# Kernel optimization log

Measured on AMD Instinct MI355X. Metric: run time of the kernel, lower is better.

The kernel has to match this reference:

```python
import jax, jax.numpy as jnp
import numpy as np

NUM_EXPERTS = 64
TOP_K = 2
B, S, EMB, MLP = 4, 2048, 1024, 2048


def setup_inputs() -> dict:
    key = jax.random.key(0)
    k1, k2, k3, k4, k5 = jax.random.split(key, 5)
    inputs = jax.random.normal(k1, (B, S, EMB), dtype=jnp.float32)
    gate_kernel = jax.random.normal(k2, (EMB, NUM_EXPERTS), dtype=jnp.float32) / np.sqrt(EMB)
    w0 = jax.random.normal(k3, (NUM_EXPERTS, EMB, MLP), dtype=jnp.float32) / np.sqrt(EMB)
    w1 = jax.random.normal(k4, (NUM_EXPERTS, EMB, MLP), dtype=jnp.float32) / np.sqrt(EMB)
    wo = jax.random.normal(k5, (NUM_EXPERTS, MLP, EMB), dtype=jnp.float32) / np.sqrt(MLP)
    return {"inputs": inputs, "gate_kernel": gate_kernel, "w0": w0, "w1": w1, "wo": wo}


def reference(inputs, gate_kernel, w0, w1, wo):
    b, s, e = inputs.shape
    x = inputs.reshape(b * s, e)                                  # [T, E]
    # Router (DenseGeneral gate)
    gate_logits = jnp.einsum('te,ex->tx', x, gate_kernel)         # [T, X]
    # permute(): top-k gating + sort tokens by expert
    weights, selected = jax.lax.top_k(gate_logits, TOP_K)         # [T, K]
    weights = jax.nn.softmax(weights.astype(jnp.float32), axis=-1)
    flat_experts = selected.reshape(-1)                           # [T*K]
    sort_idx = jnp.argsort(flat_experts)                          # [T*K]
    token_idx = sort_idx // TOP_K
    sorted_x = jnp.take(x, token_idx, axis=0)                     # [T*K, E]
    group_sizes = jnp.bincount(flat_experts, length=NUM_EXPERTS).astype(jnp.int32)
    # grouped GEMMs (gated FFN: silu(x@w0) * (x@w1) @ wo)
    h0 = jax.lax.ragged_dot(sorted_x, w0, group_sizes)            # [T*K, M]
    h1 = jax.lax.ragged_dot(sorted_x, w1, group_sizes)            # [T*K, M]
    inter = jax.nn.silu(h0) * h1
    out_sorted = jax.lax.ragged_dot(inter, wo, group_sizes)       # [T*K, E]
    # unpermute(): restore token order, weighted combine over top-k
    unsorted = jnp.take(out_sorted, jnp.argsort(sort_idx), axis=0)
    per_tok = unsorted.reshape(b * s, TOP_K, e)
    out = jnp.einsum('BKE,BK->BE', per_tok.astype(jnp.float32), weights)
    return out.reshape(b, s, e)
```

## Files before the change

kernel.cpp:

```cpp
#include <hip/hip_runtime.h>
#include <hip/hip_bf16.h>
#include <math.h>

#define NTOK   8192
#define NEXP   64
#define EMBD   1024
#define MLPD   2048
#define TOPK   2
#define NFLAT  (NTOK * TOPK)
#define BKD    32
#define MAXCH  8

typedef __attribute__((ext_vector_type(4)))  float  f32x4;
typedef __attribute__((ext_vector_type(16))) float  f32x16;
typedef __attribute__((ext_vector_type(8)))  __bf16 bf16x8;

__device__ __forceinline__ void gl16(const void* g, void* lds_base) {
  __builtin_amdgcn_global_load_lds(
      (const __attribute__((address_space(1))) unsigned int*)g,
      (__attribute__((address_space(3))) unsigned int*)lds_base, 16, 0, 0);
}
__device__ __forceinline__ void vm0_bar() {
  asm volatile("s_waitcnt vmcnt(0)" ::: "memory");
  __builtin_amdgcn_s_barrier();
}
__device__ __forceinline__ void lgkm0_bar() {
  asm volatile("s_waitcnt lgkmcnt(0)" ::: "memory");
  __builtin_amdgcn_sched_barrier(0);
  __builtin_amdgcn_s_barrier();
}

#define OFF_COUNTS 0
#define OFF_BASE   256
#define OFF_RUN    512
#define OFF_EFLAT  1024
#define OFF_WFLAT  (1024 + 65536)
#define OFF_ROWTOK (1024 + 2 * 65536)
#define OFF_F2R    (1024 + 3 * 65536)
#define OFF_INTER  (1024 + 4 * 65536)
#define OFF_OS     (OFF_INTER + (size_t)NFLAT * MLPD * 2)
#define NEED_F32   (OFF_OS + (size_t)NFLAT * EMBD * 4)

__global__ __launch_bounds__(256) void router_topk(
    const float* __restrict__ x, const float* __restrict__ gk,
    int* __restrict__ e_flat, float* __restrict__ w_flat) {
  int t = blockIdx.x * 4 + (threadIdx.x >> 6);
  int l = threadIdx.x & 63;
  const float* xr = x + (size_t)t * EMBD;
  float acc = 0.f;
  #pragma unroll 8
  for (int i = 0; i < EMBD; ++i)
    acc = fmaf(xr[i], gk[i * NEXP + l], acc);
  float m = acc;
  for (int o = 32; o; o >>= 1) m = fmaxf(m, __shfl_xor(m, o));
  unsigned long long b1 = __ballot(acc == m);
  int i1 = __ffsll(b1) - 1;
  float v2 = (l == i1) ? -INFINITY : acc;
  float m2 = v2;
  for (int o = 32; o; o >>= 1) m2 = fmaxf(m2, __shfl_xor(m2, o));
  unsigned long long b2 = __ballot(v2 == m2);
  int i2 = __ffsll(b2) - 1;
  if (l == 0) {
    float e2 = expf(m2 - m);
    float inv = 1.f / (1.f + e2);
    e_flat[2 * t] = i1;  e_flat[2 * t + 1] = i2;
    w_flat[2 * t] = inv; w_flat[2 * t + 1] = e2 * inv;
  }
}

__global__ void hist_k(const int* __restrict__ ef, int* __restrict__ counts) {
  int j = blockIdx.x * 256 + threadIdx.x;
  if (j < NFLAT) atomicAdd(&counts[ef[j]], 1);
}

__global__ void scan_k(const int* __restrict__ counts, int* __restrict__ base) {
  if (threadIdx.x == 0) {
    int s = 0;
    for (int e = 0; e < NEXP; ++e) { base[e] = s; s += counts[e]; }
  }
}

__global__ void scatter_k(const int* __restrict__ ef, const int* __restrict__ base,
                          int* __restrict__ run, int* __restrict__ rowtok,
                          int* __restrict__ f2r) {
  int j = blockIdx.x * 256 + threadIdx.x;
  if (j < NFLAT) {
    int e = ef[j];
    int r = base[e] + atomicAdd(&run[e], 1);
    f2r[j] = r;
    rowtok[r] = j >> 1;
  }
}

__global__ __launch_bounds__(256, 3) void gemm1_k(
    const float* __restrict__ x, const float* __restrict__ w0,
    const float* __restrict__ w1, const int* __restrict__ counts,
    const int* __restrict__ base, const int* __restrict__ rowtok,
    __hip_bfloat16* __restrict__ inter) {
  int e = blockIdx.z;
  int Me = counts[e];
  int mc = blockIdx.y;
  if (mc * 128 >= Me) return;
  int rs = base[e];
  int nb = blockIdx.x * 64;
  int t = threadIdx.x;
  int wv = t >> 6, l = t & 63;
  int wr = wv >> 1, wc = wv & 1;
  int lo = l & 31, hi = l >> 5;

  __shared__ float Ash[4096];
  __shared__ float Bsh[2 * 2048];

  const float* abase0 = x;
  const float* abase1 = x;
  const float* wbase  = w0;
  if (wv < 2) {
    int g0 = wv * 2, g1 = wv * 2 + 1;
    int r0 = mc * 128 + g0 * 32 + lo; r0 = r0 < Me ? r0 : Me - 1;
    int r1 = mc * 128 + g1 * 32 + lo; r1 = r1 < Me ? r1 : Me - 1;
    abase0 = x + (size_t)rowtok[rs + r0] * EMBD + hi * 4;
    abase1 = x + (size_t)rowtok[rs + r1] * EMBD + hi * 4;
  } else {
    const float* w = (wv == 3) ? w1 : w0;
    wbase = w + (size_t)e * EMBD * MLPD + nb + (l & 15) * 4 + (size_t)(l >> 4) * MLPD;
  }
  int matofs = (wv & 1) * 2048;

  auto STAGE = [&](int kk) {
    if (wv < 2) {
      #pragma unroll
      for (int h = 0; h < 4; ++h) {
        gl16(abase0 + kk + h * 8, &Ash[((wv * 2 + 0) * 4 + h) * 256]);
        gl16(abase1 + kk + h * 8, &Ash[((wv * 2 + 1) * 4 + h) * 256]);
      }
    } else {
      #pragma unroll
      for (int j = 0; j < 8; ++j)
        gl16(wbase + (size_t)(kk + j * 4) * MLPD, &Bsh[matofs + j * 256]);
    }
  };

  f32x16 acc0[2], acc1[2];
  #pragma unroll
  for (int g = 0; g < 2; ++g)
    #pragma unroll
    for (int r = 0; r < 16; ++r) { acc0[g][r] = 0.f; acc1[g][r] = 0.f; }

  STAGE(0);
  const int NT = EMBD / BKD;
  for (int ks = 0; ks < NT; ++ks) {
    vm0_bar();
    f32x4 a[2][2][2];
    #pragma unroll
    for (int g = 0; g < 2; ++g)
      #pragma unroll
      for (int kh = 0; kh < 2; ++kh) {
        int idx = (((wr * 2 + g) * 4 + kh * 2 + hi) * 256) + lo * 4;
        a[g][kh][0] = *(const f32x4*)&Ash[idx];
        a[g][kh][1] = *(const f32x4*)&Ash[idx + 128];
      }
    float b[2][2][8];
    #pragma unroll
    for (int m = 0; m < 2; ++m)
      #pragma unroll
      for (int kh = 0; kh < 2; ++kh) {
        int bi = m * 2048 + (kh * 16 + hi * 8) * 64 + wc * 32 + lo;
        #pragma unroll
        for (int q = 0; q < 8; ++q) b[m][kh][q] = Bsh[bi + q * 64];
      }
    lgkm0_bar();
    if (ks + 1 < NT) STAGE((ks + 1) * BKD);
    bf16x8 av[2][2], bv[2][2];
    #pragma unroll
    for (int g = 0; g < 2; ++g)
      #pragma unroll
      for (int kh = 0; kh < 2; ++kh) {
        #pragma unroll
        for (int q = 0; q < 4; ++q) {
          av[g][kh][q]     = (__bf16)a[g][kh][0][q];
          av[g][kh][4 + q] = (__bf16)a[g][kh][1][q];
        }
      }
    #pragma unroll
    for (int m = 0; m < 2; ++m)
      #pragma unroll
      for (int kh = 0; kh < 2; ++kh)
        #pragma unroll
        for (int q = 0; q < 8; ++q) bv[m][kh][q] = (__bf16)b[m][kh][q];
    #pragma unroll
    for (int kh = 0; kh < 2; ++kh)
      #pragma unroll
      for (int g = 0; g < 2; ++g) {
        acc0[g] = __builtin_amdgcn_mfma_f32_32x32x16_bf16(av[g][kh], bv[0][kh], acc0[g], 0, 0, 0);
        acc1[g] = __builtin_amdgcn_mfma_f32_32x32x16_bf16(av[g][kh], bv[1][kh], acc1[g], 0, 0, 0);
      }
  }

  #pragma unroll
  for (int g = 0; g < 2; ++g)
    #pragma unroll
    for (int r = 0; r < 16; ++r) {
      int rl = mc * 128 + wr * 64 + g * 32 + (r & 3) + 8 * (r >> 2) + 4 * hi;
      if (rl < Me) {
        float h0 = acc0[g][r], h1 = acc1[g][r];
        float s = h0 / (1.f + expf(-h0)) * h1;
        inter[(size_t)(rs + rl) * MLPD + nb + wc * 32 + lo] = (__hip_bfloat16)s;
      }
    }
}

template <typename OS_T>
__global__ __launch_bounds__(256, 4) void gemm2_k(
    const __hip_bfloat16* __restrict__ inter, const float* __restrict__ wo,
    const int* __restrict__ counts, const int* __restrict__ base,
    OS_T* __restrict__ os) {
  int e = blockIdx.z;
  int Me = counts[e];
  int mc = blockIdx.y;
  if (mc * 128 >= Me) return;
  int rs = base[e];
  int nb = blockIdx.x * 64;
  int t = threadIdx.x;
  int wv = t >> 6, l = t & 63;
  int wr = wv >> 1, wc = wv & 1;
  int lo = l & 31, hi = l >> 5;

  __shared__ __bf16 A2[4096];
  __shared__ float  B2[2048];

  const __hip_bfloat16* ab0 = inter;
  const __hip_bfloat16* ab1 = inter;
  const float* wbase = wo;
  if (wv < 2) {
    int g0 = wv * 2, g1 = wv * 2 + 1;
    int r0 = mc * 128 + g0 * 32 + lo; r0 = r0 < Me ? r0 : Me - 1;
    int r1 = mc * 128 + g1 * 32 + lo; r1 = r1 < Me ? r1 : Me - 1;
    ab0 = inter + (size_t)(rs + r0) * MLPD + hi * 8;
    ab1 = inter + (size_t)(rs + r1) * MLPD + hi * 8;
  } else {
    wbase = wo + (size_t)e * MLPD * EMBD + nb + (l & 15) * 4 + (size_t)(l >> 4) * EMBD;
  }
  int jofs = (wv & 1) * 4;

  auto STAGE = [&](int kk) {
    if (wv < 2) {
      #pragma unroll
      for (int kh = 0; kh < 2; ++kh) {
        gl16(ab0 + kk + kh * 16, &A2[((wv * 2 + 0) * 2 + kh) * 512]);
        gl16(ab1 + kk + kh * 16, &A2[((wv * 2 + 1) * 2 + kh) * 512]);
      }
    } else {
      #pragma unroll
      for (int j = 0; j < 4; ++j)
        gl16(wbase + (size_t)(kk + (jofs + j) * 4) * EMBD, &B2[(jofs + j) * 256]);
    }
  };

  f32x16 acc[2];
  #pragma unroll
  for (int g = 0; g < 2; ++g)
    #pragma unroll
    for (int r = 0; r < 16; ++r) acc[g][r] = 0.f;

  STAGE(0);
  const int NT = MLPD / BKD;
  for (int ks = 0; ks < NT; ++ks) {
    vm0_bar();
    bf16x8 av[2][2];
    #pragma unroll
    for (int g = 0; g < 2; ++g)
      #pragma unroll
      for (int kh = 0; kh < 2; ++kh)
        av[g][kh] = *(const bf16x8*)&A2[(((wr * 2 + g) * 2 + kh) * 512) + l * 8];
    float b[2][8];
    #pragma unroll
    for (int kh = 0; kh < 2; ++kh) {
      int bi = (kh * 16 + hi * 8) * 64 + wc * 32 + lo;
      #pragma unroll
      for (int q = 0; q < 8; ++q) b[kh][q] = B2[bi + q * 64];
    }
    lgkm0_bar();
    if (ks + 1 < NT) STAGE((ks + 1) * BKD);
    bf16x8 bv[2];
    #pragma unroll
    for (int kh = 0; kh < 2; ++kh)
      #pragma unroll
      for (int q = 0; q < 8; ++q) bv[kh][q] = (__bf16)b[kh][q];
    #pragma unroll
    for (int kh = 0; kh < 2; ++kh)
      #pragma unroll
      for (int g = 0; g < 2; ++g)
        acc[g] = __builtin_amdgcn_mfma_f32_32x32x16_bf16(av[g][kh], bv[kh], acc[g], 0, 0, 0);
  }

  #pragma unroll
  for (int g = 0; g < 2; ++g)
    #pragma unroll
    for (int r = 0; r < 16; ++r) {
      int rl = mc * 128 + wr * 64 + g * 32 + (r & 3) + 8 * (r >> 2) + 4 * hi;
      if (rl < Me)
        os[(size_t)(rs + rl) * EMBD + nb + wc * 32 + lo] = (OS_T)acc[g][r];
    }
}

template <typename OS_T>
__global__ __launch_bounds__(256) void combine_k(
    const OS_T* __restrict__ os, const int* __restrict__ f2r,
    const float* __restrict__ wf, float* __restrict__ out) {
  int t = blockIdx.x;
  int c = threadIdx.x * 4;
  int r0 = f2r[2 * t], r1 = f2r[2 * t + 1];
  float wa = wf[2 * t], wb = wf[2 * t + 1];
  const OS_T* pa = os + (size_t)r0 * EMBD + c;
  const OS_T* pb = os + (size_t)r1 * EMBD + c;
  float4 o;
  o.x = wa * (float)pa[0] + wb * (float)pb[0];
  o.y = wa * (float)pa[1] + wb * (float)pb[1];
  o.z = wa * (float)pa[2] + wb * (float)pb[2];
  o.w = wa * (float)pa[3] + wb * (float)pb[3];
  *(float4*)(out + (size_t)t * EMBD + c) = o;
}

extern "C" void kernel_launch(void* const* d_in, const int* in_sizes, int n_in,
                              void* d_out, int out_size, void* d_ws, size_t ws_size,
                              hipStream_t stream) {
  const float* x  = (const float*)d_in[0];
  const float* gk = (const float*)d_in[1];
  const float* w0 = (const float*)d_in[2];
  const float* w1 = (const float*)d_in[3];
  const float* wo = (const float*)d_in[4];
  float* out = (float*)d_out;
  char* ws = (char*)d_ws;

  int*   counts = (int*)(ws + OFF_COUNTS);
  int*   basep  = (int*)(ws + OFF_BASE);
  int*   run    = (int*)(ws + OFF_RUN);
  int*   ef     = (int*)(ws + OFF_EFLAT);
  float* wfl    = (float*)(ws + OFF_WFLAT);
  int*   rowtok = (int*)(ws + OFF_ROWTOK);
  int*   f2r    = (int*)(ws + OFF_F2R);
  __hip_bfloat16* inter = (__hip_bfloat16*)(ws + OFF_INTER);

  hipMemsetAsync(ws, 0, 1024, stream);
  router_topk<<<NTOK / 4, 256, 0, stream>>>(x, gk, ef, wfl);
  hist_k<<<NFLAT / 256, 256, 0, stream>>>(ef, counts);
  scan_k<<<1, 64, 0, stream>>>(counts, basep);
  scatter_k<<<NFLAT / 256, 256, 0, stream>>>(ef, basep, run, rowtok, f2r);
  gemm1_k<<<dim3(MLPD / 64, MAXCH, NEXP), 256, 0, stream>>>(x, w0, w1, counts, basep, rowtok, inter);

  if (ws_size >= NEED_F32) {
    float* os = (float*)(ws + OFF_OS);
    gemm2_k<float><<<dim3(EMBD / 64, MAXCH, NEXP), 256, 0, stream>>>(inter, wo, counts, basep, os);
    combine_k<float><<<NTOK, 256, 0, stream>>>(os, f2r, wfl, out);
  } else {
    __hip_bfloat16* os = (__hip_bfloat16*)(ws + OFF_OS);
    gemm2_k<__hip_bfloat16><<<dim3(EMBD / 64, MAXCH, NEXP), 256, 0, stream>>>(inter, wo, counts, basep, os);
    combine_k<__hip_bfloat16><<<NTOK, 256, 0, stream>>>(os, f2r, wfl, out);
  }
}
```

Measured before the change: 1.098 ms.

## Double-buffer weight tiles in LDS with partial vmcnt waits in both GEMMs

Adds a second LDS buffer for the weight tiles in gemm1, and for both the A and B tiles in gemm2, and prefetches two K-steps ahead. Waits become partial (vmcnt(8) or vmcnt(4)) instead of a full drain, so global-to-LDS loads for the next tile overlap the current step's compute. The cost is more LDS per block, which may lower occupancy (gemm1's B buffer grows to 32KB). The per-wave vmcnt counting also has to stay correct for the prefetch to be safe.

```diff
diff --git a/kernel.cpp b/kernel.cpp
--- a/kernel.cpp
+++ b/kernel.cpp
@@ -19,10 +19,6 @@
   __builtin_amdgcn_global_load_lds(
       (const __attribute__((address_space(1))) unsigned int*)g,
       (__attribute__((address_space(3))) unsigned int*)lds_base, 16, 0, 0);
-}
-__device__ __forceinline__ void vm0_bar() {
-  asm volatile("s_waitcnt vmcnt(0)" ::: "memory");
-  __builtin_amdgcn_s_barrier();
 }
 __device__ __forceinline__ void lgkm0_bar() {
   asm volatile("s_waitcnt lgkmcnt(0)" ::: "memory");
@@ -109,7 +105,7 @@
   int lo = l & 31, hi = l >> 5;
 
   __shared__ float Ash[4096];
-  __shared__ float Bsh[2 * 2048];
+  __shared__ float Bsh[2][4096];
 
   const float* abase0 = x;
   const float* abase1 = x;
@@ -126,18 +122,17 @@
   }
   int matofs = (wv & 1) * 2048;
 
-  auto STAGE = [&](int kk) {
-    if (wv < 2) {
-      #pragma unroll
-      for (int h = 0; h < 4; ++h) {
-        gl16(abase0 + kk + h * 8, &Ash[((wv * 2 + 0) * 4 + h) * 256]);
-        gl16(abase1 + kk + h * 8, &Ash[((wv * 2 + 1) * 4 + h) * 256]);
-      }
-    } else {
-      #pragma unroll
-      for (int j = 0; j < 8; ++j)
-        gl16(wbase + (size_t)(kk + j * 4) * MLPD, &Bsh[matofs + j * 256]);
-    }
+  auto STAGE_A = [&](int kk) {
+    #pragma unroll
+    for (int h = 0; h < 4; ++h) {
+      gl16(abase0 + kk + h * 8, &Ash[((wv * 2 + 0) * 4 + h) * 256]);
+      gl16(abase1 + kk + h * 8, &Ash[((wv * 2 + 1) * 4 + h) * 256]);
+    }
+  };
+  auto STAGE_B = [&](int buf, int kk) {
+    #pragma unroll
+    for (int j = 0; j < 8; ++j)
+      gl16(wbase + (size_t)(kk + j * 4) * MLPD, &Bsh[buf][matofs + j * 256]);
   };
 
   f32x16 acc0[2], acc1[2];
@@ -146,10 +141,15 @@
     #pragma unroll
     for (int r = 0; r < 16; ++r) { acc0[g][r] = 0.f; acc1[g][r] = 0.f; }
 
-  STAGE(0);
+  if (wv < 2) STAGE_A(0);
+  else { STAGE_B(0, 0); STAGE_B(1, BKD); }
+
   const int NT = EMBD / BKD;
   for (int ks = 0; ks < NT; ++ks) {
-    vm0_bar();
+    if (wv >= 2 && ks + 1 < NT) asm volatile("s_waitcnt vmcnt(8)" ::: "memory");
+    else                        asm volatile("s_waitcnt vmcnt(0)" ::: "memory");
+    __builtin_amdgcn_s_barrier();
+
     f32x4 a[2][2][2];
     #pragma unroll
     for (int g = 0; g < 2; ++g)
@@ -160,27 +160,29 @@
         a[g][kh][1] = *(const f32x4*)&Ash[idx + 128];
       }
     float b[2][2][8];
+    const float* bb = Bsh[ks & 1];
     #pragma unroll
     for (int m = 0; m < 2; ++m)
       #pragma unroll
       for (int kh = 0; kh < 2; ++kh) {
         int bi = m * 2048 + (kh * 16 + hi * 8) * 64 + wc * 32 + lo;
         #pragma unroll
-        for (int q = 0; q < 8; ++q) b[m][kh][q] = Bsh[bi + q * 64];
+        for (int q = 0; q < 8; ++q) b[m][kh][q] = bb[bi + q * 64];
       }
     lgkm0_bar();
-    if (ks + 1 < NT) STAGE((ks + 1) * BKD);
+    if (wv < 2) { if (ks + 1 < NT) STAGE_A((ks + 1) * BKD); }
+    else if (ks + 2 < NT) STAGE_B(ks & 1, (ks + 2) * BKD);
+
     bf16x8 av[2][2], bv[2][2];
     #pragma unroll
     for (int g = 0; g < 2; ++g)
       #pragma unroll
-      for (int kh = 0; kh < 2; ++kh) {
+      for (int kh = 0; kh < 2; ++kh)
         #pragma unroll
         for (int q = 0; q < 4; ++q) {
           av[g][kh][q]     = (__bf16)a[g][kh][0][q];
           av[g][kh][4 + q] = (__bf16)a[g][kh][1][q];
         }
-      }
     #pragma unroll
     for (int m = 0; m < 2; ++m)
       #pragma unroll
@@ -225,8 +227,8 @@
   int wr = wv >> 1, wc = wv & 1;
   int lo = l & 31, hi = l >> 5;
 
-  __shared__ __bf16 A2[4096];
-  __shared__ float  B2[2048];
+  __shared__ __bf16 A2[2][4096];
+  __shared__ float  B2[2][2048];
 
   const __hip_bfloat16* ab0 = inter;
   const __hip_bfloat16* ab1 = inter;
@@ -242,17 +244,17 @@
   }
   int jofs = (wv & 1) * 4;
 
-  auto STAGE = [&](int kk) {
+  auto STAGE = [&](int buf, int kk) {
     if (wv < 2) {
       #pragma unroll
       for (int kh = 0; kh < 2; ++kh) {
-        gl16(ab0 + kk + kh * 16, &A2[((wv * 2 + 0) * 2 + kh) * 512]);
-        gl16(ab1 + kk + kh * 16, &A2[((wv * 2 + 1) * 2 + kh) * 512]);
+        gl16(ab0 + kk + kh * 16, &A2[buf][((wv * 2 + 0) * 2 + kh) * 512]);
+        gl16(ab1 + kk + kh * 16, &A2[buf][((wv * 2 + 1) * 2 + kh) * 512]);
       }
     } else {
       #pragma unroll
       for (int j = 0; j < 4; ++j)
-        gl16(wbase + (size_t)(kk + (jofs + j) * 4) * EMBD, &B2[(jofs + j) * 256]);
+        gl16(wbase + (size_t)(kk + (jofs + j) * 4) * EMBD, &B2[buf][(jofs + j) * 256]);
     }
   };
 
@@ -262,25 +264,30 @@
     #pragma unroll
     for (int r = 0; r < 16; ++r) acc[g][r] = 0.f;
 
-  STAGE(0);
+  STAGE(0, 0);
+  STAGE(1, BKD);
   const int NT = MLPD / BKD;
   for (int ks = 0; ks < NT; ++ks) {
-    vm0_bar();
+    if (ks + 1 < NT) asm volatile("s_waitcnt vmcnt(4)" ::: "memory");
+    else             asm volatile("s_waitcnt vmcnt(0)" ::: "memory");
+    __builtin_amdgcn_s_barrier();
+
     bf16x8 av[2][2];
     #pragma unroll
     for (int g = 0; g < 2; ++g)
       #pragma unroll
       for (int kh = 0; kh < 2; ++kh)
-        av[g][kh] = *(const bf16x8*)&A2[(((wr * 2 + g) * 2 + kh) * 512) + l * 8];
+        av[g][kh] = *(const bf16x8*)&A2[ks & 1][(((wr * 2 + g) * 2 + kh) * 512) + l * 8];
     float b[2][8];
     #pragma unroll
     for (int kh = 0; kh < 2; ++kh) {
       int bi = (kh * 16 + hi * 8) * 64 + wc * 32 + lo;
       #pragma unroll
-      for (int q = 0; q < 8; ++q) b[kh][q] = B2[bi + q * 64];
+      for (int q = 0; q < 8; ++q) b[kh][q] = B2[ks & 1][bi + q * 64];
     }
     lgkm0_bar();
-    if (ks + 1 < NT) STAGE((ks + 1) * BKD);
+    if (ks + 2 < NT) STAGE(ks & 1, (ks + 2) * BKD);
+
     bf16x8 bv[2];
     #pragma unroll
     for (int kh = 0; kh < 2; ++kh)
```

Measured after the change: 1.087 ms. Within noise of the previous version (-1.0%).
